# Performance work log

Measured on AMD Instinct MI355X. Metric: run time of the kernel, lower is better.

The kernel has to match this reference:

```python
import jax, jax.numpy as jnp
import numpy as np
from jax import lax

B, N, C, CN, M, H, W = 2, 8192, 64, 64, 16, 180, 240
LN_EPS = 1e-5  # torch nn.LayerNorm([C]) default eps


def setup_inputs():
    key = jax.random.key(0)
    ks = jax.random.split(key, 20)
    x = jax.random.uniform(ks[0], (B, N)) * (W - 1)
    y = jax.random.uniform(ks[1], (B, N)) * (H - 1)
    t = jax.random.uniform(ks[2], (B, N))
    p = jnp.where(jax.random.uniform(ks[3], (B, N)) < 0.5, -1.0, 1.0)
    events = jnp.stack([x, y, t, p], axis=-1)  # [B,N,4]
    s = 0.05
    w = lambda k, shape: jax.random.normal(k, shape) * s
    return {
        "events": events,
        "W_mlp1": w(ks[4], (4, C)),
        "W_pe": w(ks[5], (4, CN)),
        "ln_w": jnp.ones((C,)),
        "ln_b": jnp.zeros((C,)),
        "lx_Wq": w(ks[6], (C, CN)), "lx_Wk": w(ks[7], (C, CN)),
        "lx_Wv": w(ks[8], (C, CN)), "lx_Wsa1": w(ks[9], (CN, 1)),
        "lx_Wsa2": w(ks[10], (CN, C)),
        "gx_Wq": w(ks[11], (C, CN)), "gx_Wk": w(ks[12], (C, CN)),
        "gx_Wv": w(ks[13], (C, CN)), "gx_Wpe": w(ks[14], (C, CN)),
        "gx_Wsa1": w(ks[15], (CN, 1)), "gx_Wsa2": w(ks[16], (CN, C)),
    }


def select_nearest(vect, m):
    # torch: F.pad(left=m//2, right=m//2-1) then unfold(dim=1, size=m, step=1)
    b, n, c = vect.shape
    pad = m // 2
    vp = jnp.pad(vect, ((0, 0), (pad, pad - 1), (0, 0)))
    idx = jnp.arange(n)[:, None] + jnp.arange(m)[None, :]  # [N,M]
    return vp[:, idx, :]  # [B,N,M,C]


def fps(event, npoint):
    # faithful farthest_point_sample_batch; masked_select returns the sampled
    # points in ORIGINAL index order, hence the sort of selected indices.
    b, n, c = event.shape
    bary = jnp.mean(event, axis=1, keepdims=True)
    farthest0 = jnp.argmax(jnp.sum((event - bary) ** 2, -1), axis=1)  # [B]
    dist0 = jnp.full((b, n), 1e10, event.dtype)

    def step(carry, _):
        distance, farthest = carry
        centroid = jnp.take_along_axis(event, farthest[:, None, None], axis=1)
        d = jnp.sum((event - centroid) ** 2, -1)
        distance = jnp.minimum(distance, d)  # distance[dist<distance]=dist
        return (distance, jnp.argmax(distance, axis=1)), farthest

    _, sel = lax.scan(step, (dist0, farthest0), None, length=npoint)
    sel = jnp.sort(sel.T, axis=1)  # [B,npoint], sorted index order
    return jnp.take_along_axis(event, sel[:, :, None], axis=1)  # [B,npoint,C]


def sub_attention(q, k_multi, v_multi, pe, Wsa1, Wsa2):
    # sa = q - k + pe -> Linear(Cn,1) -> softmax over M.
    # The original then computes matmul(scores[B,1,N,M], (v+pe)^T[B,Cn,M,N])
    # and sums over the last axis, which is exactly
    #   scores @ (sum_n (v_multi + pe))  -- computed here without the
    # [B,Cn,N,N] intermediate.
    sa = q[:, :, None, :] - k_multi + pe          # [B,N,M,Cn]
    logits = jnp.squeeze(sa @ Wsa1, -1)           # [B,N,M]
    scores = jax.nn.softmax(logits, axis=-1)
    S = jnp.sum(v_multi + pe, axis=1)             # [B,M,Cn]
    p_attn = jnp.einsum("bnm,bmc->bnc", scores, S)
    return p_attn @ Wsa2                          # [B,N,C]


def layer_norm(x, w, b):
    mu = jnp.mean(x, axis=-1, keepdims=True)
    var = jnp.var(x, axis=-1, keepdims=True)
    return (x - mu) / jnp.sqrt(var + LN_EPS) * w + b


def normalize_nonzero(space):
    # mean/std over nonzero entries (std unbiased, ddof=1 as torch.std)
    mask = space != 0
    cnt = jnp.sum(mask)
    mean = jnp.sum(jnp.where(mask, space, 0.0)) / jnp.maximum(cnt, 1)
    var = jnp.sum(jnp.where(mask, (space - mean) ** 2, 0.0)) / jnp.maximum(cnt - 1, 1)
    std = jnp.sqrt(var)
    centered = jnp.where(mask, space - mean, space)
    safe_std = jnp.where(std > 0, std, 1.0)
    normed = jnp.where(std > 0, centered / safe_std, centered)
    return jnp.where(cnt > 0, normed, space)


def events_to_image(feat, ev, ln_w, ln_b):
    # feat [N,C], ev [N,4]
    h = jax.nn.gelu(layer_norm(feat, ln_w, ln_b), approximate=False)
    xi = jnp.floor(ev[:, 0]).astype(jnp.int32)
    yi = jnp.floor(ev[:, 1]).astype(jnp.int32)
    p = ev[:, 3]
    flat = yi * W + xi
    space = jnp.zeros((H * W, h.shape[1]), h.dtype).at[flat].add(p[:, None] * h)
    return normalize_nonzero(space.reshape(H, W, -1))


def reference(events, W_mlp1, W_pe, ln_w, ln_b,
              lx_Wq, lx_Wk, lx_Wv, lx_Wsa1, lx_Wsa2,
              gx_Wq, gx_Wk, gx_Wv, gx_Wpe, gx_Wsa1, gx_Wsa2):
    b, n, _ = events.shape
    lx_in = events @ W_mlp1                                    # [B,N,C]
    # EventTransformer position encoding: unfold-neighbor differences in raw
    # 4-d event space, then Linear(4,Cn)
    pe = (events[:, :, None, :] - select_nearest(events, M)) @ W_pe  # [B,N,M,Cn]
    # LXformer
    q = lx_in @ lx_Wq
    k = lx_in @ lx_Wk
    v = lx_in @ lx_Wv
    lx_sa = sub_attention(q, select_nearest(k, M), select_nearest(v, M),
                          pe, lx_Wsa1, lx_Wsa2)
    lx_out = lx_in + lx_sa
    # GXformer: FPS-sampled global keys/values, FPS-based position encoding
    pe_g = (lx_out[:, :, None, :] - fps(lx_out, M)[:, None, :, :]) @ gx_Wpe
    qg = lx_out @ gx_Wq
    kg = lx_out @ gx_Wk
    vg = lx_out @ gx_Wv
    k_m = jnp.broadcast_to(fps(kg, M)[:, None], (b, n, M, CN))
    v_m = jnp.broadcast_to(fps(vg, M)[:, None], (b, n, M, CN))
    gx_sa = sub_attention(qg, k_m, v_m, pe_g, gx_Wsa1, gx_Wsa2)
    gx_out = lx_out + gx_sa
    # scatter events to image per batch element
    imgs = jax.vmap(lambda f, e: events_to_image(f, e, ln_w, ln_b))(gx_out, events)
    return jnp.transpose(imgs, (0, 3, 1, 2))  # [B,C,H,W]
```

## Files before the change

kernel.cpp:

```cpp
#include <hip/hip_runtime.h>


typedef unsigned short u16;
typedef unsigned long long ull;

#define NB 8192
#define IMG_H 180
#define IMG_W 240
#define HWPIX (IMG_H*IMG_W)
#define SPB (HWPIX*64)
#define NC (NB*64)

#define TT_AC    0
#define TT_T     16384
#define TT_W1    32768
#define TT_EDGEV 32960
#define TT_EDGEF 35008
#define TT_S     37056
#define TT_SEL   39104
#define TT_CG    45248
#define TT_ESUM  45376
#define TT_STATS 45408
#define TT_SYNC  45440
#define TT_GCNT  45632
#define TT_LXS   45664
#define TT_ZOFF  45376
#define TT_ZCNT  416
#define TT_TOT   45792

__device__ __forceinline__ float bf2f(u16 u){
  union { unsigned int i; float f; } w; w.i = ((unsigned int)u) << 16; return w.f;
}
__device__ __forceinline__ u16 f2bf(float f){
  union { unsigned int i; float f; } w; w.f = f;
  unsigned int x = w.i;
  x += 0x7fffu + ((x >> 16) & 1u);
  return (u16)(x >> 16);
}
__device__ __forceinline__ bool isbf(const void* ev){
  unsigned w3 = ((const unsigned*)ev)[3];
  return !(w3 == 0x3F800000u || w3 == 0xBF800000u);
}
__device__ __forceinline__ float ld(const void* p, int i, bool bf){
  return bf ? bf2f(((const u16*)p)[i]) : ((const float*)p)[i];
}
__device__ __forceinline__ void stout(void* o, long i, float v, bool bf){
  if (bf) ((u16*)o)[i] = f2bf(v); else ((float*)o)[i] = v;
}
__device__ __forceinline__ float waveSum(float v){
#pragma unroll
  for (int m = 1; m < 64; m <<= 1) v += __shfl_xor(v, m, 64);
  return v;
}
__device__ __forceinline__ ull waveMaxU64(ull v){
#pragma unroll
  for (int m = 1; m < 64; m <<= 1){
    ull o = (ull)__shfl_xor((long long)v, m, 64);
    if (o > v) v = o;
  }
  return v;
}
__device__ __forceinline__ ull packPDI(int phase, float d, int n){
  return ((ull)phase << 45) | ((ull)__float_as_uint(d) << 13) | (ull)(8191 - n);
}
__device__ __forceinline__ int unpackI(ull p){ return 8191 - (int)(p & 0x1FFFull); }

__global__ void kW(const void* __restrict__ ev, const void* __restrict__ Wq,
                   const void* __restrict__ Wk, const void* __restrict__ Wpe,
                   const void* __restrict__ w1, float* __restrict__ ws, int tail){
  const bool bf = isbf(ev);
  const int tid = threadIdx.x;
  for (int i = tid; i < TT_ZCNT; i += 256) ws[tail + TT_ZOFF + i] = 0.f;
  if (tid < 64){
    float s1 = 0.f, s2 = 0.f;
    for (int c = 0; c < 64; c++){
      float wc = ld(w1, c, bf);
      s1 += ld(Wq, tid*64 + c, bf) * wc;
      s2 += ld(Wk, tid*64 + c, bf) * wc;
    }
    ws[tail + TT_W1 + tid] = s1;
    ws[tail + TT_W1 + 64 + tid] = s2;
    if (tid < 4){
      float s3 = 0.f;
      for (int c = 0; c < 64; c++) s3 += ld(Wpe, tid*64 + c, bf) * ld(w1, c, bf);
      ws[tail + TT_W1 + 128 + tid] = s3;
    }
  }
}

__global__ void __launch_bounds__(256, 4) kA(const void* __restrict__ ev,
    const void* __restrict__ Wm, const void* __restrict__ Wpe,
    const void* __restrict__ Wv, float* __restrict__ ws,
    int offA, int strA, int tail, int bb0){
  const bool bf = isbf(ev);
  const int bb = bb0 + blockIdx.z;
  const int lane = threadIdx.x & 63, w = threadIdx.x >> 6;
  float* A = ws + offA + (size_t)bb*strA;
  const float wq1 = ws[tail + TT_W1 + lane];
  const float wk1 = ws[tail + TT_W1 + 64 + lane];
  const float wp10 = ws[tail+TT_W1+128], wp11 = ws[tail+TT_W1+129],
              wp12 = ws[tail+TT_W1+130], wp13 = ws[tail+TT_W1+131];
  const float wm0 = ld(Wm, 0*64+lane, bf), wm1 = ld(Wm, 1*64+lane, bf),
              wm2 = ld(Wm, 2*64+lane, bf), wm3 = ld(Wm, 3*64+lane, bf);
  const bool edgeBlk = (blockIdx.x == 0 || blockIdx.x == 1023);
  float se0 = 0.f, se1 = 0.f, se2 = 0.f, se3 = 0.f;
#pragma unroll
  for (int i = 0; i < 2; i++){
    const int n = blockIdx.x*8 + w + 4*i;
    const int e4 = (bb*NB + n)*4;
    float e0 = ld(ev, e4+0, bf), e1 = ld(ev, e4+1, bf),
          e2 = ld(ev, e4+2, bf), e3 = ld(ev, e4+3, bf);
    se0 += e0; se1 += e1; se2 += e2; se3 += e3;
    float lx = e0*wm0 + e1*wm1 + e2*wm2 + e3*wm3;
    float epe = e0*wp10 + e1*wp11 + e2*wp12 + e3*wp13;
    float acv = waveSum(lx * wq1) + epe;
    float tv  = waveSum(lx * wk1) + epe;
    A[n*64 + lane] = lx;
    if (lane == 0){
      ws[tail + TT_AC + bb*8192 + n] = acv;
      ws[tail + TT_T  + bb*8192 + n] = tv;
    }
    if (edgeBlk && (n < 8 || n >= NB-8)){
      int e = (n < 8) ? n : (n - (NB-16));
      float v = 0.f;
      for (int cn = 0; cn < 64; cn++)
        v += __shfl(lx, cn, 64) * ld(Wv, cn*64 + lane, bf);
      float f = e0*ld(Wpe, lane, bf) + e1*ld(Wpe, 64+lane, bf)
              + e2*ld(Wpe, 128+lane, bf) + e3*ld(Wpe, 192+lane, bf);
      ws[tail + TT_EDGEV + bb*1024 + e*64 + lane] = v;
      ws[tail + TT_EDGEF + bb*1024 + e*64 + lane] = f;
    }
  }
  __shared__ float esum[4][4];
  if (lane == 0){ esum[w][0]=se0; esum[w][1]=se1; esum[w][2]=se2; esum[w][3]=se3; }
  __syncthreads();
  if (threadIdx.x < 4)
    atomicAdd(&ws[tail + TT_ESUM + bb*16 + threadIdx.x],
              esum[0][threadIdx.x]+esum[1][threadIdx.x]+esum[2][threadIdx.x]+esum[3][threadIdx.x]);
}

__global__ void __launch_bounds__(64) kB(const void* __restrict__ ev,
    const void* __restrict__ Wm, const void* __restrict__ Wv,
    const void* __restrict__ Wsa2, float* __restrict__ ws, int tail, int bb0){
  const bool bf = isbf(ev);
  const int bb = bb0 + blockIdx.z;
  const int m = blockIdx.x, lane = threadIdx.x;
  float tm = 0.f;
#pragma unroll
  for (int i = 0; i < 4; i++) tm += ws[tail + TT_ESUM + bb*16 + i] * ld(Wm, i*64 + lane, bf);
  float vs0 = 0.f, vs1 = 0.f;
#pragma unroll
  for (int j = 0; j < 64; j += 2){
    vs0 += __shfl(tm, j, 64)   * ld(Wv, j*64 + lane, bf);
    vs1 += __shfl(tm, j+1, 64) * ld(Wv, (j+1)*64 + lane, bf);
  }
  float vsum = vs0 + vs1;
  const int d = m - 8;
  float sv = 0.f, sf = 0.f;
  const float* EV = ws + tail + TT_EDGEV + bb*1024;
  const float* EF = ws + tail + TT_EDGEF + bb*1024;
  if (d < 0){
    for (int e = 16 + d; e < 16; e++){ sv += EV[e*64+lane]; sf += EF[e*64+lane]; }
  } else {
    for (int e = 0; e < d; e++){ sv += EV[e*64+lane]; sf += EF[e*64+lane]; }
  }
  float S = vsum - sv + sf;
  float sw0 = 0.f, sw1 = 0.f;
#pragma unroll
  for (int c = 0; c < 64; c += 2){
    sw0 += __shfl(S, c, 64)   * ld(Wsa2, c*64 + lane, bf);
    sw1 += __shfl(S, c+1, 64) * ld(Wsa2, (c+1)*64 + lane, bf);
  }
  ws[tail + TT_S + bb*1024 + m*64 + lane] = sw0 + sw1;
}

__global__ void __launch_bounds__(256) kC(const void* __restrict__ ev,
    const void* __restrict__ gWk, const void* __restrict__ gWv,
    float* __restrict__ ws,
    int offA, int strA, int offB, int strB, int offC, int strC,
    int tail, int bb0){
  const bool bf = isbf(ev);
  const int bb = bb0 + blockIdx.z;
  float* A = ws + offA + (size_t)bb*strA;
  float* Bp = ws + offB + (size_t)bb*strB;
  float* Cp = ws + offC + (size_t)bb*strC;
  __shared__ float SW_lds[1024];
  __shared__ float WK[4096];
  __shared__ float WV[4096];
  __shared__ __align__(16) float LXU[8*64 + 8*16];
  const int tid = threadIdx.x, lane = tid & 63, w = tid >> 6;
  float* LX  = LXU;
  float* SIG = LXU + 512;
  for (int i = tid; i < 1024; i += 256) SW_lds[i] = ws[tail + TT_S + bb*1024 + i];
  for (int i = tid; i < 4096; i += 256){
    WK[i] = ld(gWk, i, bf);
    WV[i] = ld(gWv, i, bf);
  }
  __syncthreads();
  float lxsum = 0.f;
#pragma unroll
  for (int i = 0; i < 2; i++){
    const int p = w + 4*i;
    const int n = blockIdx.x*8 + p;
    float lx  = A[n*64 + lane];
    float acn = ws[tail + TT_AC + bb*8192 + n];
    const int m = lane & 15;
    const int j = n + m - 8;
    float tv = (j >= 0 && j < NB) ? ws[tail + TT_T + bb*8192 + j] : 0.f;
    float logit = acn - tv;
    float mx = logit;
#pragma unroll
    for (int k = 1; k < 16; k <<= 1) mx = fmaxf(mx, __shfl_xor(mx, k, 64));
    float ex = expf(logit - mx);
    float sm = ex;
#pragma unroll
    for (int k = 1; k < 16; k <<= 1) sm += __shfl_xor(sm, k, 64);
    float sig = ex / sm;
    if (lane < 16) SIG[p*16 + lane] = sig;
    float sa = 0.f;
#pragma unroll
    for (int mm = 0; mm < 16; mm += 4){
      float4 s4 = *(const float4*)&SIG[p*16 + mm];
      sa += s4.x*SW_lds[ mm   *64+lane] + s4.y*SW_lds[(mm+1)*64+lane]
          + s4.z*SW_lds[(mm+2)*64+lane] + s4.w*SW_lds[(mm+3)*64+lane];
    }
    float lxo = lx + sa;
    LX[p*64 + lane] = lxo;
    Bp[n*64 + lane] = lxo;
    lxsum += lxo;
  }
#pragma unroll
  for (int i = 0; i < 2; i++){
    const int p = w + 4*i;
    const int n = blockIdx.x*8 + p;
    float k0 = 0.f, v0 = 0.f;
#pragma unroll
    for (int cn = 0; cn < 64; cn += 4){
      float4 x4 = *(const float4*)&LX[p*64 + cn];
      k0 += x4.x*WK[ cn   *64+lane] + x4.y*WK[(cn+1)*64+lane]
          + x4.z*WK[(cn+2)*64+lane] + x4.w*WK[(cn+3)*64+lane];
      v0 += x4.x*WV[ cn   *64+lane] + x4.y*WV[(cn+1)*64+lane]
          + x4.z*WV[(cn+2)*64+lane] + x4.w*WV[(cn+3)*64+lane];
    }
    A[n*64 + lane] = k0;
    Cp[n*64 + lane] = v0;
  }
  __syncthreads();
  float* lred = LXU;
  lred[w*64 + lane] = lxsum;
  __syncthreads();
  if (tid < 64)
    atomicAdd(&ws[tail + TT_LXS + bb*64 + tid],
              lred[tid]+lred[64+tid]+lred[128+tid]+lred[192+tid]);
}

__global__ void __launch_bounds__(512) kFPS(const void* __restrict__ ev,
    const void* __restrict__ gWk, const void* __restrict__ gWv,
    const void* __restrict__ gWpe, const void* __restrict__ gWsa1,
    const void* __restrict__ gWsa2, float* __restrict__ ws,
    int offA, int strA, int offB, int strB, int offC, int strC,
    int offSp, int strSp, int tail, int bb0){
  const int g = blockIdx.y, idx = blockIdx.x;
  const int bb = bb0 + blockIdx.z;
  const int tid = threadIdx.x, lane = tid & 63, w = tid >> 6;

  if (g == 3){
    float4 z = make_float4(0.f, 0.f, 0.f, 0.f);
    size_t base; unsigned cnt4;
    if (blockIdx.z == 0){ base = (size_t)offSp + 4u*NC; cnt4 = (SPB - 4*NC)/4; }
    else                { base = (size_t)offSp + (size_t)strSp; cnt4 = SPB/4; }
    float4* p = (float4*)(ws + base);
    for (unsigned i = idx*512u + tid; i < cnt4; i += 8u*512u) p[i] = z;
    return;
  }

  const float* pts = ws + (g == 0 ? offB + (size_t)bb*strB
                         : g == 1 ? offA + (size_t)bb*strA
                                  : offC + (size_t)bb*strC);
  ull* slot = (ull*)(ws + tail + TT_SYNC + (bb*3 + g)*32);
  int* gcnt = (int*)(ws + tail + TT_GCNT + bb*16);

  __shared__ float cent[64];
  __shared__ float lxsS[64];
  __shared__ ull   wvS[8];
  __shared__ int   selS[16];
  __shared__ int   sCur;
  __shared__ float gfS[1024];
  __shared__ float betaS[16];
  __shared__ float GS[64];

  const int n0 = idx*1024 + tid;
  float4 P[2][16];
#pragma unroll
  for (int j = 0; j < 2; j++)
#pragma unroll
    for (int i = 0; i < 16; i++)
      P[j][i] = ((const float4*)(pts + (size_t)(n0 + j*512)*64))[i];

  const bool bf = isbf(ev);
  if (tid < 64){
    float lxs = ws[tail + TT_LXS + bb*64 + tid];
    lxsS[tid] = lxs;
    float c;
    if (g == 0) c = lxs * (1.0f/NB);
    else {
      const void* W = (g == 1) ? gWk : gWv;
      float s = 0.f;
#pragma unroll
      for (int j = 0; j < 64; j++) s += __shfl(lxs, j, 64) * ld(W, j*64 + tid, bf);
      c = s * (1.0f/NB);
    }
    cent[tid] = c;
  }
  __syncthreads();

  const float4* cv = (const float4*)cent;
  float md[2] = {1e10f, 1e10f};
  int cur;

  {
    float dd[2];
#pragma unroll
    for (int j = 0; j < 2; j++){
      float d = 0.f;
#pragma unroll
      for (int i = 0; i < 16; i++){
        float4 c = cv[i];
        float dx = P[j][i].x-c.x, dy = P[j][i].y-c.y, dz = P[j][i].z-c.z, dw = P[j][i].w-c.w;
        d += dx*dx; d += dy*dy; d += dz*dz; d += dw*dw;
      }
      dd[j] = d;
    }
    ull p0 = packPDI(1, dd[0], n0);
    ull p1 = packPDI(1, dd[1], n0 + 512);
    ull bp = waveMaxU64(p0 > p1 ? p0 : p1);
    if (lane == 0) wvS[w] = bp;
    __syncthreads();
    if (w == 0){
      ull v = (lane < 8) ? wvS[lane] : 0;
#pragma unroll
      for (int m = 1; m < 8; m <<= 1){
        ull o = (ull)__shfl_xor((long long)v, m, 64);
        if (o > v) v = o;
      }
      if (lane == 0)
        __hip_atomic_store(&slot[8 + idx], v, __ATOMIC_RELEASE, __HIP_MEMORY_SCOPE_AGENT);
      ull got;
      for (;;){
        got = (lane < 8) ? __hip_atomic_load(&slot[8 + lane], __ATOMIC_RELAXED, __HIP_MEMORY_SCOPE_AGENT) : 0;
        ull ok = __ballot(lane >= 8 || (int)(got >> 45) == 1);
        if (ok == ~0ull) break;
        __builtin_amdgcn_s_sleep(1);
      }
#pragma unroll
      for (int m = 1; m < 8; m <<= 1){
        ull o = (ull)__shfl_xor((long long)got, m, 64);
        if (o > got) got = o;
      }
      if (lane == 0) sCur = unpackI(got);
    }
    __syncthreads();
    cur = sCur;
  }

  for (int it = 0; ; it++){
    if (tid == 0) selS[it] = cur;
    if (it == 15) break;
    if (tid < 16) ((float4*)cent)[tid] = ((const float4*)(pts + (size_t)cur*64))[tid];
    __syncthreads();
    const int phase = it + 2;
    float dd[2];
#pragma unroll
    for (int j = 0; j < 2; j++){
      float d = 0.f;
#pragma unroll
      for (int i = 0; i < 16; i++){
        float4 c = cv[i];
        float dx = P[j][i].x-c.x, dy = P[j][i].y-c.y, dz = P[j][i].z-c.z, dw = P[j][i].w-c.w;
        d += dx*dx; d += dy*dy; d += dz*dz; d += dw*dw;
      }
      md[j] = fminf(md[j], d);
      dd[j] = md[j];
    }
    ull p0 = packPDI(phase, dd[0], n0);
    ull p1 = packPDI(phase, dd[1], n0 + 512);
    ull bp = waveMaxU64(p0 > p1 ? p0 : p1);
    if (lane == 0) wvS[w] = bp;
    __syncthreads();
    const int par = phase & 1;
    if (w == 0){
      ull v = (lane < 8) ? wvS[lane] : 0;
#pragma unroll
      for (int m = 1; m < 8; m <<= 1){
        ull o = (ull)__shfl_xor((long long)v, m, 64);
        if (o > v) v = o;
      }
      if (lane == 0)
        __hip_atomic_store(&slot[par*8 + idx], v, __ATOMIC_RELEASE, __HIP_MEMORY_SCOPE_AGENT);
      ull got;
      for (;;){
        got = (lane < 8) ? __hip_atomic_load(&slot[par*8 + lane], __ATOMIC_RELAXED, __HIP_MEMORY_SCOPE_AGENT) : 0;
        ull ok = __ballot(lane >= 8 || (int)(got >> 45) == phase);
        if (ok == ~0ull) break;
        __builtin_amdgcn_s_sleep(1);
      }
#pragma unroll
      for (int m = 1; m < 8; m <<= 1){
        ull o = (ull)__shfl_xor((long long)got, m, 64);
        if (o > got) got = o;
      }
      if (lane == 0) sCur = unpackI(got);
    }
    __syncthreads();
    cur = sCur;
  }
  __syncthreads();

  if (idx == 0){
    if (tid == 0){
      for (int i = 1; i < 16; i++){
        int key = selS[i]; int j = i - 1;
        while (j >= 0 && selS[j] > key){ selS[j+1] = selS[j]; j--; }
        selS[j+1] = key;
      }
    }
    __syncthreads();
    for (int idx2 = tid; idx2 < 1024; idx2 += 512)
      ws[tail + TT_SEL + bb*3072 + g*1024 + idx2] = pts[(size_t)selS[idx2 >> 6]*64 + (idx2 & 63)];
    __threadfence();
  }
  __syncthreads();
  if (tid == 0) atomicAdd(gcnt, 1);
  if (g != 0 || idx != 0) return;

  if (tid == 0){
    while (__hip_atomic_load(gcnt, __ATOMIC_RELAXED, __HIP_MEMORY_SCOPE_AGENT) < 24)
      __builtin_amdgcn_s_sleep(1);
    __threadfence();
  }
  __syncthreads();
  if (tid < 64){
    const float gw1 = ld(gWsa1, tid, bf);
    float wpec[64];
#pragma unroll
    for (int cn = 0; cn < 64; cn++) wpec[cn] = ld(gWpe, cn*64 + tid, bf);
    float lxs = lxsS[tid];
    float G = 0.f;
#pragma unroll
    for (int cn = 0; cn < 64; cn++) G += __shfl(lxs, cn, 64) * wpec[cn];
    GS[tid] = G;
    const float* selp = ws + tail + TT_SEL + bb*3072;
    for (int m = 0; m < 16; m++){
      float plx = selp[m*64 + tid];
      float g2 = 0.f;
#pragma unroll
      for (int cn = 0; cn < 64; cn++) g2 += __shfl(plx, cn, 64) * wpec[cn];
      gfS[m*64 + tid] = g2;
      float pkv = selp[1024 + m*64 + tid];
      float part = waveSum((pkv + g2) * gw1);
      if (tid == 0) betaS[m] = part;
    }
  }
  __syncthreads();
  if (tid < 64){
    float mx = -1e30f;
    for (int m = 0; m < 16; m++) mx = fmaxf(mx, -betaS[m]);
    float ssum = 0.f;
    for (int m = 0; m < 16; m++) ssum += expf(-betaS[m] - mx);
    float A = 0.f;
    for (int m = 0; m < 16; m++){
      float sg = expf(-betaS[m] - mx) / ssum;
      float pv = ws[tail + TT_SEL + bb*3072 + 2048 + m*64 + tid];
      float Sg = 8192.0f * (pv - gfS[m*64 + tid]) + GS[tid];
      A += sg * Sg;
    }
    float cg = 0.f;
#pragma unroll
    for (int cn = 0; cn < 64; cn++) cg += __shfl(A, cn, 64) * ld(gWsa2, cn*64 + tid, bf);
    ws[tail + TT_CG + bb*64 + tid] = cg;
  }
}

__global__ void kZero(float* __restrict__ ws, int base, unsigned count4){
  unsigned i = blockIdx.x*256u + threadIdx.x;
  if (i < count4)
    ((float4*)(ws + base))[i] = make_float4(0.f, 0.f, 0.f, 0.f);
}

__global__ void __launch_bounds__(256, 4) kImg(const void* __restrict__ ev,
    const void* __restrict__ lnw, const void* __restrict__ lnb,
    float* __restrict__ ws, int offB, int strB, int offSp, int strSp,
    int tail, int bb0){
  const bool bf = isbf(ev);
  const int bb = bb0 + blockIdx.z;
  const int lane = threadIdx.x & 63, w = threadIdx.x >> 6;
  const float cg = ws[tail + TT_CG + bb*64 + lane];
  const float lw = ld(lnw, lane, bf), lb = ld(lnb, lane, bf);
  float* space = ws + offSp + (size_t)bb*strSp;
  const float* Bp = ws + offB + (size_t)bb*strB;
#pragma unroll
  for (int i = 0; i < 2; i++){
    const int n = blockIdx.x*8 + w + 4*i;
    float x = Bp[n*64 + lane] + cg;
    float mu = waveSum(x) * (1.0f/64.0f);
    float dv = x - mu;
    float var = waveSum(dv*dv) * (1.0f/64.0f);
    float xn = dv / sqrtf(var + 1e-5f);
    float y = xn * lw + lb;
    float h = 0.5f * y * (1.0f + erff(y * 0.70710678118654752f));
    const int e4 = (bb*NB + n)*4;
    float exf = ld(ev, e4+0, bf), eyf = ld(ev, e4+1, bf), epf = ld(ev, e4+3, bf);
    int xi = (int)floorf(exf), yi = (int)floorf(eyf);
    int flat = yi*IMG_W + xi;
    flat = max(0, min(HWPIX-1, flat));
    atomicAdd(space + flat*64 + lane, epf * h);
  }
}

__global__ void __launch_bounds__(256) kStat(float* __restrict__ ws,
    int offSp, int strSp, int tail, int bb0){
  const int bb = bb0 + blockIdx.z;
  const float4* sp = (const float4*)(ws + offSp + (size_t)bb*strSp);
  float cnt = 0.f, sum = 0.f, ssq = 0.f;
  for (unsigned i = blockIdx.x*256u + threadIdx.x; i < SPB/4; i += 65536u){
    float4 v = sp[i];
    if (v.x != 0.f){ cnt += 1.f; sum += v.x; ssq += v.x*v.x; }
    if (v.y != 0.f){ cnt += 1.f; sum += v.y; ssq += v.y*v.y; }
    if (v.z != 0.f){ cnt += 1.f; sum += v.z; ssq += v.z*v.z; }
    if (v.w != 0.f){ cnt += 1.f; sum += v.w; ssq += v.w*v.w; }
  }
  cnt = waveSum(cnt); sum = waveSum(sum); ssq = waveSum(ssq);
  __shared__ float rc[4], rs[4], rq[4];
  const int lane = threadIdx.x & 63, w = threadIdx.x >> 6;
  if (lane == 0){ rc[w] = cnt; rs[w] = sum; rq[w] = ssq; }
  __syncthreads();
  if (threadIdx.x == 0){
    atomicAdd(&ws[tail + TT_STATS + bb*16 + 0], rc[0]+rc[1]+rc[2]+rc[3]);
    atomicAdd(&ws[tail + TT_STATS + bb*16 + 1], rs[0]+rs[1]+rs[2]+rs[3]);
    atomicAdd(&ws[tail + TT_STATS + bb*16 + 2], rq[0]+rq[1]+rq[2]+rq[3]);
  }
}

__global__ void __launch_bounds__(256) kOut(const void* __restrict__ ev,
    const float* __restrict__ ws, void* __restrict__ out,
    int offSp, int strSp, int tail, int bb0){
  const bool bf = isbf(ev);
  const int bb = bb0 + blockIdx.z;
  __shared__ float tile[64*65];
  const int tid = threadIdx.x;
  const int hw0 = blockIdx.x*64;
  const float* sp = ws + offSp + (size_t)bb*strSp;
#pragma unroll
  for (int i = 0; i < 16; i++){
    int idx = tid + 256*i;
    tile[(idx >> 6)*65 + (idx & 63)] = sp[(size_t)hw0*64 + idx];
  }
  const float cnt = ws[tail + TT_STATS + bb*16 + 0];
  const float sum = ws[tail + TT_STATS + bb*16 + 1];
  const float ssq = ws[tail + TT_STATS + bb*16 + 2];
  const float mean = sum / fmaxf(cnt, 1.f);
  const float m2   = fmaxf(ssq - sum*mean, 0.f);
  const float var  = m2 / fmaxf(cnt - 1.f, 1.f);
  const float stdv = sqrtf(var);
  __syncthreads();
  const int c = tid >> 2, sub = tid & 3;
#pragma unroll
  for (int j = 0; j < 16; j++){
    int hwl = sub*16 + j;
    float x = tile[hwl*65 + c];
    float centered = (x != 0.f) ? (x - mean) : x;
    float normed = (stdv > 0.f) ? (centered / stdv) : centered;
    float o = (cnt > 0.f) ? normed : x;
    stout(out, (long)(bb*64 + c)*HWPIX + hw0 + hwl, o, bf);
  }
}

extern "C" void kernel_launch(void* const* d_in, const int* in_sizes, int n_in,
                              void* d_out, int out_size, void* d_ws, size_t ws_size,
                              hipStream_t stream){
  (void)in_sizes; (void)n_in; (void)out_size;
  const void* ev     = d_in[0];
  const void* Wm     = d_in[1];
  const void* Wpe    = d_in[2];
  const void* lnw    = d_in[3];
  const void* lnb    = d_in[4];
  const void* lxWq   = d_in[5];
  const void* lxWk   = d_in[6];
  const void* lxWv   = d_in[7];
  const void* lxWsa1 = d_in[8];
  const void* lxWsa2 = d_in[9];
  const void* gxWk   = d_in[11];
  const void* gxWv   = d_in[12];
  const void* gxWpe  = d_in[13];
  const void* gxWsa1 = d_in[14];
  const void* gxWsa2 = d_in[15];
  float* ws = (float*)d_ws;

  const int P_TAIL = 2*NC + 2*SPB;
  const size_t PAR_BYTES = (size_t)(P_TAIL + TT_TOT) * 4;
  const bool par = ws_size >= PAR_BYTES;

  int offB, strB, offSp, strSp, offA, strA, offC, strC, tail;
  if (par){
    offB = 0;        strB = NC;
    offSp = 2*NC;    strSp = SPB;
    offA = 2*NC;     strA = NC;
    offC = 4*NC;     strC = NC;
    tail = P_TAIL;
  } else {
    offSp = 0;       strSp = 0;
    offA = 0;        strA = 0;
    offC = NC;       strC = 0;
    offB = SPB;      strB = 0;
    tail = SPB + NC;
  }
  const int nb = par ? 2 : 1;
  const int iters = par ? 1 : 2;

  kW<<<1, 256, 0, stream>>>(ev, lxWq, lxWk, Wpe, lxWsa1, ws, tail);
  for (int t = 0; t < iters; t++){
    const int bb0 = par ? 0 : t;
    kA<<<dim3(1024,1,nb), 256, 0, stream>>>(ev, Wm, Wpe, lxWv, ws, offA, strA, tail, bb0);
    kB<<<dim3(16,1,nb), 64, 0, stream>>>(ev, Wm, lxWv, lxWsa2, ws, tail, bb0);
    kC<<<dim3(1024,1,nb), 256, 0, stream>>>(ev, gxWk, gxWv, ws,
        offA, strA, offB, strB, offC, strC, tail, bb0);
    kFPS<<<dim3(8, par ? 4 : 3, nb), 512, 0, stream>>>(ev, gxWk, gxWv, gxWpe, gxWsa1, gxWsa2, ws,
        offA, strA, offB, strB, offC, strC, offSp, strSp, tail, bb0);
    if (par)
      kZero<<<dim3(2048,1,1), 256, 0, stream>>>(ws, offSp, (unsigned)NC);
    else
      kZero<<<dim3(2700,1,1), 256, 0, stream>>>(ws, offSp, (unsigned)(SPB/4));
    kImg<<<dim3(1024,1,nb), 256, 0, stream>>>(ev, lnw, lnb, ws, offB, strB, offSp, strSp, tail, bb0);
    kStat<<<dim3(256,1,nb), 256, 0, stream>>>(ws, offSp, strSp, tail, bb0);
    kOut<<<dim3(675,1,nb), 256, 0, stream>>>(ev, ws, d_out, offSp, strSp, tail, bb0);
  }
}
```

Measured before the change: 325.7 us.

## Fuse kB into kC and add non-aliased workspace layout to drop kZero

Removes the small kB kernel and recomputes its 16x64 sub-attention output table inside every kC block, writing it directly to LDS instead of global memory. When the workspace is large enough, a new layout places the image scatter buffer after all feature buffers so the FPS kernel's idle group can zero the whole image buffer, skipping the separate kZero launch. This trades two launches and a serialization point for redundant per-block matvec work in kC and a larger workspace footprint.

After: 425.0 us. 30.5% more time.

```diff
diff --git a/kernel.cpp b/kernel.cpp
--- a/kernel.cpp
+++ b/kernel.cpp
@@ -139,42 +139,9 @@
               esum[0][threadIdx.x]+esum[1][threadIdx.x]+esum[2][threadIdx.x]+esum[3][threadIdx.x]);
 }
 
-__global__ void __launch_bounds__(64) kB(const void* __restrict__ ev,
-    const void* __restrict__ Wm, const void* __restrict__ Wv,
-    const void* __restrict__ Wsa2, float* __restrict__ ws, int tail, int bb0){
-  const bool bf = isbf(ev);
-  const int bb = bb0 + blockIdx.z;
-  const int m = blockIdx.x, lane = threadIdx.x;
-  float tm = 0.f;
-#pragma unroll
-  for (int i = 0; i < 4; i++) tm += ws[tail + TT_ESUM + bb*16 + i] * ld(Wm, i*64 + lane, bf);
-  float vs0 = 0.f, vs1 = 0.f;
-#pragma unroll
-  for (int j = 0; j < 64; j += 2){
-    vs0 += __shfl(tm, j, 64)   * ld(Wv, j*64 + lane, bf);
-    vs1 += __shfl(tm, j+1, 64) * ld(Wv, (j+1)*64 + lane, bf);
-  }
-  float vsum = vs0 + vs1;
-  const int d = m - 8;
-  float sv = 0.f, sf = 0.f;
-  const float* EV = ws + tail + TT_EDGEV + bb*1024;
-  const float* EF = ws + tail + TT_EDGEF + bb*1024;
-  if (d < 0){
-    for (int e = 16 + d; e < 16; e++){ sv += EV[e*64+lane]; sf += EF[e*64+lane]; }
-  } else {
-    for (int e = 0; e < d; e++){ sv += EV[e*64+lane]; sf += EF[e*64+lane]; }
-  }
-  float S = vsum - sv + sf;
-  float sw0 = 0.f, sw1 = 0.f;
-#pragma unroll
-  for (int c = 0; c < 64; c += 2){
-    sw0 += __shfl(S, c, 64)   * ld(Wsa2, c*64 + lane, bf);
-    sw1 += __shfl(S, c+1, 64) * ld(Wsa2, (c+1)*64 + lane, bf);
-  }
-  ws[tail + TT_S + bb*1024 + m*64 + lane] = sw0 + sw1;
-}
-
 __global__ void __launch_bounds__(256) kC(const void* __restrict__ ev,
+    const void* __restrict__ Wm, const void* __restrict__ lxWv,
+    const void* __restrict__ Wsa2,
     const void* __restrict__ gWk, const void* __restrict__ gWv,
     float* __restrict__ ws,
     int offA, int strA, int offB, int strB, int offC, int strC,
@@ -191,7 +158,39 @@
   const int tid = threadIdx.x, lane = tid & 63, w = tid >> 6;
   float* LX  = LXU;
   float* SIG = LXU + 512;
-  for (int i = tid; i < 1024; i += 256) SW_lds[i] = ws[tail + TT_S + bb*1024 + i];
+  {
+    float tm = 0.f;
+#pragma unroll
+    for (int i = 0; i < 4; i++) tm += ws[tail + TT_ESUM + bb*16 + i] * ld(Wm, i*64 + lane, bf);
+    float vs0 = 0.f, vs1 = 0.f;
+#pragma unroll
+    for (int j = 0; j < 64; j += 2){
+      vs0 += __shfl(tm, j, 64)   * ld(lxWv, j*64 + lane, bf);
+      vs1 += __shfl(tm, j+1, 64) * ld(lxWv, (j+1)*64 + lane, bf);
+    }
+    const float vsum = vs0 + vs1;
+    const float* EV = ws + tail + TT_EDGEV + bb*1024;
+    const float* EF = ws + tail + TT_EDGEF + bb*1024;
+#pragma unroll
+    for (int q = 0; q < 4; q++){
+      const int m = w + 4*q;
+      const int d = m - 8;
+      float sv = 0.f, sf = 0.f;
+      if (d < 0){
+        for (int e = 16 + d; e < 16; e++){ sv += EV[e*64+lane]; sf += EF[e*64+lane]; }
+      } else {
+        for (int e = 0; e < d; e++){ sv += EV[e*64+lane]; sf += EF[e*64+lane]; }
+      }
+      float S = vsum - sv + sf;
+      float sw0 = 0.f, sw1 = 0.f;
+#pragma unroll
+      for (int c = 0; c < 64; c += 2){
+        sw0 += __shfl(S, c, 64)   * ld(Wsa2, c*64 + lane, bf);
+        sw1 += __shfl(S, c+1, 64) * ld(Wsa2, (c+1)*64 + lane, bf);
+      }
+      SW_lds[m*64 + lane] = sw0 + sw1;
+    }
+  }
   for (int i = tid; i < 4096; i += 256){
     WK[i] = ld(gWk, i, bf);
     WV[i] = ld(gWv, i, bf);
@@ -259,7 +258,7 @@
     const void* __restrict__ gWpe, const void* __restrict__ gWsa1,
     const void* __restrict__ gWsa2, float* __restrict__ ws,
     int offA, int strA, int offB, int strB, int offC, int strC,
-    int offSp, int strSp, int tail, int bb0){
+    int offSp, int strSp, int fullZero, int tail, int bb0){
   const int g = blockIdx.y, idx = blockIdx.x;
   const int bb = bb0 + blockIdx.z;
   const int tid = threadIdx.x, lane = tid & 63, w = tid >> 6;
@@ -267,8 +266,9 @@
   if (g == 3){
     float4 z = make_float4(0.f, 0.f, 0.f, 0.f);
     size_t base; unsigned cnt4;
-    if (blockIdx.z == 0){ base = (size_t)offSp + 4u*NC; cnt4 = (SPB - 4*NC)/4; }
-    else                { base = (size_t)offSp + (size_t)strSp; cnt4 = SPB/4; }
+    if (fullZero){ base = (size_t)offSp + (size_t)blockIdx.z*strSp; cnt4 = SPB/4; }
+    else if (blockIdx.z == 0){ base = (size_t)offSp + 4u*NC; cnt4 = (SPB - 4*NC)/4; }
+    else { base = (size_t)offSp + (size_t)strSp; cnt4 = SPB/4; }
     float4* p = (float4*)(ws + base);
     for (unsigned i = idx*512u + tid; i < cnt4; i += 8u*512u) p[i] = z;
     return;
@@ -596,12 +596,19 @@
   const void* gxWsa2 = d_in[15];
   float* ws = (float*)d_ws;
 
-  const int P_TAIL = 2*NC + 2*SPB;
-  const size_t PAR_BYTES = (size_t)(P_TAIL + TT_TOT) * 4;
-  const bool par = ws_size >= PAR_BYTES;
+  const int P2_TAIL = 6*NC + 2*SPB;
+  const int P_TAIL  = 2*NC + 2*SPB;
+  const bool par2 = ws_size >= (size_t)(P2_TAIL + TT_TOT) * 4;
+  const bool par  = par2 || ws_size >= (size_t)(P_TAIL + TT_TOT) * 4;
 
   int offB, strB, offSp, strSp, offA, strA, offC, strC, tail;
-  if (par){
+  if (par2){
+    offB = 0;        strB = NC;
+    offA = 2*NC;     strA = NC;
+    offC = 4*NC;     strC = NC;
+    offSp = 6*NC;    strSp = SPB;
+    tail = P2_TAIL;
+  } else if (par){
     offB = 0;        strB = NC;
     offSp = 2*NC;    strSp = SPB;
     offA = 2*NC;     strA = NC;
@@ -621,15 +628,16 @@
   for (int t = 0; t < iters; t++){
     const int bb0 = par ? 0 : t;
     kA<<<dim3(1024,1,nb), 256, 0, stream>>>(ev, Wm, Wpe, lxWv, ws, offA, strA, tail, bb0);
-    kB<<<dim3(16,1,nb), 64, 0, stream>>>(ev, Wm, lxWv, lxWsa2, ws, tail, bb0);
-    kC<<<dim3(1024,1,nb), 256, 0, stream>>>(ev, gxWk, gxWv, ws,
+    kC<<<dim3(1024,1,nb), 256, 0, stream>>>(ev, Wm, lxWv, lxWsa2, gxWk, gxWv, ws,
         offA, strA, offB, strB, offC, strC, tail, bb0);
     kFPS<<<dim3(8, par ? 4 : 3, nb), 512, 0, stream>>>(ev, gxWk, gxWv, gxWpe, gxWsa1, gxWsa2, ws,
-        offA, strA, offB, strB, offC, strC, offSp, strSp, tail, bb0);
-    if (par)
-      kZero<<<dim3(2048,1,1), 256, 0, stream>>>(ws, offSp, (unsigned)NC);
-    else
-      kZero<<<dim3(2700,1,1), 256, 0, stream>>>(ws, offSp, (unsigned)(SPB/4));
+        offA, strA, offB, strB, offC, strC, offSp, strSp, par2 ? 1 : 0, tail, bb0);
+    if (!par2){
+      if (par)
+        kZero<<<dim3(2048,1,1), 256, 0, stream>>>(ws, offSp, (unsigned)NC);
+      else
+        kZero<<<dim3(2700,1,1), 256, 0, stream>>>(ws, offSp, (unsigned)(SPB/4));
+    }
     kImg<<<dim3(1024,1,nb), 256, 0, stream>>>(ev, lnw, lnb, ws, offB, strB, offSp, strSp, tail, bb0);
     kStat<<<dim3(256,1,nb), 256, 0, stream>>>(ws, offSp, strSp, tail, bb0);
     kOut<<<dim3(675,1,nb), 256, 0, stream>>>(ev, ws, d_out, offSp, strSp, tail, bb0);
```
